# Kernel optimization log

Hardware: AMD Instinct MI355X
Metric: run time of the kernel (lower is better)

Reference implementation:

```python
import jax, jax.numpy as jnp
import numpy as np

B, T, C = 4, 2048, 1024
H, HKV, D = 8, 4, 128          # query heads, kv heads, head dim (C = H*D)
RATIO = 4                       # csa_compress_ratio -> block size
G = T // RATIO                  # number of compressed blocks (T divisible by RATIO)
HI, DI = 8, 64                  # indexer heads / head dim
TOPK = 64                       # index_topk blocks selected per query
ROPE_DIM = 64                   # partial RoPE applied to last ROPE_DIM dims of D
THETA = 160000.0                # compress_rope_theta
RANK = 512                      # grouped output projection rank (o_groups=1)
NEG = -1e30


def rmsnorm(x):
    return x * jax.lax.rsqrt(jnp.mean(jnp.square(x), axis=-1, keepdims=True) + 1e-6)


def rope_tables(pos):
    half = ROPE_DIM // 2
    inv_freq = 1.0 / (THETA ** (jnp.arange(half, dtype=jnp.float32) / half))
    ang = pos.astype(jnp.float32)[:, None] * inv_freq[None, :]   # [P, half]
    return jnp.cos(ang), jnp.sin(ang)


def partial_rope(x, cos, sin):
    # x: [..., P, heads, D]; rotate only the last ROPE_DIM dims
    x_nope, x_rope = x[..., :-ROPE_DIM], x[..., -ROPE_DIM:]
    x1, x2 = jnp.split(x_rope, 2, axis=-1)
    c = cos[:, None, :]  # [P,1,half] broadcast over heads
    s = sin[:, None, :]
    rot = jnp.concatenate([x1 * c - x2 * s, x1 * s + x2 * c], axis=-1)
    return jnp.concatenate([x_nope, rot], axis=-1)


def gated_compress(x, Wk, Wv, Wg, ape, n_head, head_dim):
    # Learned gated softmax pooling over fixed blocks of RATIO tokens.
    k = (x @ Wk).reshape(B, G, RATIO, n_head, head_dim)
    v = (x @ Wv).reshape(B, G, RATIO, n_head, head_dim)
    g = (x @ Wg).reshape(B, G, RATIO, n_head, head_dim) + ape[None, None]
    w = jax.nn.softmax(g, axis=2)
    return (k * w).sum(axis=2), (v * w).sum(axis=2)  # [B,G,h,d]


def setup_inputs() -> dict:
    key = jax.random.key(0)
    ks = jax.random.split(key, 11)
    s = 0.02
    def w(k, shape):
        return jax.random.normal(k, shape, jnp.float32) * s
    return {
        "x": jax.random.normal(ks[0], (B, T, C), jnp.float32),
        "Wq": w(ks[1], (C, H * D)),
        "Wck": w(ks[2], (C, HKV * D)),
        "Wcv": w(ks[3], (C, HKV * D)),
        "Wcg": w(ks[4], (C, HKV * D)),
        "ape_c": jnp.zeros((RATIO, HKV, D), jnp.float32),
        "Wiq": w(ks[5], (C, HI * DI)),
        "Wik": w(ks[6], (C, HI * DI)),
        "Wig": w(ks[7], (C, HI * DI)),
        "ape_i": jnp.zeros((RATIO, HI, DI), jnp.float32),
        "Wa": w(ks[8], (1, RANK, C)),
        "Wb": w(ks[9], (RANK, C)),
    }


def reference(x, Wq, Wck, Wcv, Wcg, ape_c, Wiq, Wik, Wig, ape_i, Wa, Wb):
    group_ends = jnp.arange(RATIO - 1, T, RATIO)                 # [G]
    causal = group_ends[None, :] <= jnp.arange(T)[:, None]       # [T,G]

    # --- LightningIndexer: select TOPK compressed blocks per query token ---
    ki = (x @ Wik).reshape(B, G, RATIO, HI, DI)
    gi = (x @ Wig).reshape(B, G, RATIO, HI, DI) + ape_i[None, None]
    wi = jax.nn.softmax(gi, axis=2)
    ikeys = rmsnorm((ki * wi).sum(axis=2))                       # [B,G,HI,DI]
    iq = rmsnorm((x @ Wiq).reshape(B, T, HI, DI))
    isc = jnp.einsum('bthd,bghd->bhtg', iq, ikeys) * (DI ** -0.5)
    isc = isc.mean(axis=1)                                       # [B,T,G]
    isc = jnp.where(causal[None], isc, NEG)
    sel = jax.lax.top_k(isc, TOPK)[1]                            # [B,T,TOPK]
    mask = jnp.zeros((B, T, G), dtype=bool).at[
        jnp.arange(B)[:, None, None], jnp.arange(T)[None, :, None], sel
    ].set(True)
    mask = mask & causal[None]                                   # [B,T,G]

    # --- Compressed KV + partial RoPE ---
    ck, cv = gated_compress(x, Wck, Wcv, Wcg, ape_c, HKV, D)     # [B,G,HKV,D]
    cos_q, sin_q = rope_tables(jnp.arange(T))
    cos_k, sin_k = rope_tables(group_ends)
    q = partial_rope((x @ Wq).reshape(B, T, H, D), cos_q, sin_q)
    ck = partial_rope(ck, cos_k, sin_k)

    # --- GQA attention over selected compressed blocks ---
    rep = H // HKV
    ck_r = jnp.repeat(ck, rep, axis=2)                           # [B,G,H,D]
    cv_r = jnp.repeat(cv, rep, axis=2)
    scores = jnp.einsum('bthd,bghd->bhtg', q, ck_r) * (D ** -0.5)
    m = mask[:, None]                                            # [B,1,T,G]
    attw = jax.nn.softmax(jnp.where(m, scores, NEG), axis=-1) * m
    attn = jnp.einsum('bhtg,bghd->bthd', attw, cv_r).reshape(B, T, C)

    # --- GroupedOutputProjection (o_groups=1, low-rank) ---
    r = jnp.einsum('btgd,grd->btgr', attn.reshape(B, T, 1, C), Wa).reshape(B, T, RANK)
    return rmsnorm(r) @ Wb
```

## Files before the change

kernel.cpp:

```cpp
#include <hip/hip_runtime.h>
#include <hip/hip_bf16.h>
#include <math.h>

constexpr int kB = 4, kT = 2048, kC = 1024;
constexpr int kH = 8, kHKV = 4, kD = 128;
constexpr int kRATIO = 4, kG = 512;
constexpr int kHI = 8, kDI = 64;
constexpr int kTOPK = 64, kRANK = 512;
constexpr float kTHETA = 160000.0f;
constexpr float kNEG = -1e30f;

constexpr int NTOT = 2560;
constexpr int Q_OFF = 0;
constexpr int CK_OFF = 1024;
constexpr int CV_OFF = 1536;
constexpr int CG_OFF = 2048;

constexpr int PLD = 1536;
constexpr int P_IQ = 0, P_KI = 512, P_GI = 1024;

typedef short short8 __attribute__((ext_vector_type(8)));
typedef float floatx4 __attribute__((ext_vector_type(4)));

__device__ inline float waveReduceSum(float v) {
    #pragma unroll
    for (int m = 32; m > 0; m >>= 1) v += __shfl_xor(v, m, 64);
    return v;
}
__device__ inline double waveReduceSumD(double v) {
    #pragma unroll
    for (int m = 32; m > 0; m >>= 1) v += __shfl_xor(v, m, 64);
    return v;
}
__device__ inline float waveReduceMax(float v) {
    #pragma unroll
    for (int m = 32; m > 0; m >>= 1) v = fmaxf(v, __shfl_xor(v, m, 64));
    return v;
}

__device__ inline unsigned short f2bf(float f) {
    union { float f; unsigned int u; } v; v.f = f;
    unsigned int r = v.u + 0x7FFFu + ((v.u >> 16) & 1u);
    return (unsigned short)(r >> 16);
}
__device__ inline float bf2f(unsigned short h) {
    union { unsigned int u; float f; } v; v.u = ((unsigned int)h) << 16;
    return v.f;
}

__global__ __launch_bounds__(256) void split_rows_kernel(
    const float* __restrict__ in, unsigned short* __restrict__ out,
    int K, int kshift, const float* __restrict__ rowScale)
{
    int idx = blockIdx.x * 256 + threadIdx.x;
    int row = idx >> kshift;
    int kc = (idx & ((1 << kshift) - 1)) << 2;
    float4 v = *(const float4*)(in + (size_t)row * K + kc);
    if (rowScale) {
        float s = rowScale[row];
        v.x *= s; v.y *= s; v.z *= s; v.w *= s;
    }
    unsigned short h[4], l[4];
    float vv[4] = {v.x, v.y, v.z, v.w};
    #pragma unroll
    for (int i = 0; i < 4; ++i) {
        h[i] = f2bf(vv[i]);
        l[i] = f2bf(vv[i] - bf2f(h[i]));
    }
    size_t ob = (size_t)row * (2 * K);
    uint2 hw, lw;
    hw.x = (unsigned)h[0] | ((unsigned)h[1] << 16);
    hw.y = (unsigned)h[2] | ((unsigned)h[3] << 16);
    lw.x = (unsigned)l[0] | ((unsigned)l[1] << 16);
    lw.y = (unsigned)l[2] | ((unsigned)l[3] << 16);
    *(uint2*)(out + ob + kc) = hw;
    *(uint2*)(out + ob + K + kc) = lw;
}

__global__ __launch_bounds__(256) void transpose_split_kernel(
    const float* __restrict__ W, int N, int K, unsigned short* __restrict__ Wt)
{
    __shared__ float Ws[64][68];
    int k0 = blockIdx.x * 64, n0 = blockIdx.y * 64;
    int tid = threadIdx.x;
    #pragma unroll
    for (int it = 0; it < 4; ++it) {
        int krow = (tid >> 4) + it * 16;
        float4 v = *(const float4*)(W + (size_t)(k0 + krow) * N + n0 + (tid & 15) * 4);
        *(float4*)&Ws[krow][(tid & 15) * 4] = v;
    }
    __syncthreads();
    #pragma unroll
    for (int it = 0; it < 2; ++it) {
        int idx = tid + it * 256;
        int nrow = idx >> 3;
        int kc8 = (idx & 7) * 8;
        unsigned short h[8], l[8];
        #pragma unroll
        for (int j = 0; j < 8; ++j) {
            float v = Ws[kc8 + j][nrow];
            h[j] = f2bf(v);
            l[j] = f2bf(v - bf2f(h[j]));
        }
        size_t ob = (size_t)(n0 + nrow) * (2 * K) + k0;
        uint4 hw, lw;
        hw.x = (unsigned)h[0] | ((unsigned)h[1] << 16);
        hw.y = (unsigned)h[2] | ((unsigned)h[3] << 16);
        hw.z = (unsigned)h[4] | ((unsigned)h[5] << 16);
        hw.w = (unsigned)h[6] | ((unsigned)h[7] << 16);
        lw.x = (unsigned)l[0] | ((unsigned)l[1] << 16);
        lw.y = (unsigned)l[2] | ((unsigned)l[3] << 16);
        lw.z = (unsigned)l[4] | ((unsigned)l[5] << 16);
        lw.w = (unsigned)l[6] | ((unsigned)l[7] << 16);
        *(uint4*)(Wt + ob + kc8) = hw;
        *(uint4*)(Wt + ob + K + kc8) = lw;
    }
}

#define TSTRIDE 40

__global__ __launch_bounds__(256) void gemm_mfma_kernel(
    const unsigned short* __restrict__ A,
    const unsigned short* __restrict__ B,
    float* __restrict__ C, int ldc, int Kin)
{
    __shared__ unsigned short As[128 * TSTRIDE];
    __shared__ unsigned short Bs[128 * TSTRIDE];
    const int tid = threadIdx.x;
    const int n0 = blockIdx.x * 128, m0 = blockIdx.y * 128;
    const int w = tid >> 6, lane = tid & 63;
    const int q = lane >> 4, r = lane & 15;
    const int wm = (w & 1) * 64, wn = (w >> 1) * 64;
    const int lda = 2 * Kin, ldb = 2 * Kin;
    const int srow = tid >> 2;
    const int sko = (tid & 3) * 8;

    floatx4 acc[4][4] = {};
    const int KT = 3 * Kin;
    for (int k0 = 0; k0 < KT; k0 += 32) {
        int ka = (k0 < 2 * Kin) ? k0 : k0 - 2 * Kin;
        int kb = (k0 < Kin) ? k0 : k0 - Kin;
        __syncthreads();
        #pragma unroll
        for (int rep = 0; rep < 2; ++rep) {
            int row = srow + rep * 64;
            uint4 av = *(const uint4*)(A + (size_t)(m0 + row) * lda + ka + sko);
            uint4 bv = *(const uint4*)(B + (size_t)(n0 + row) * ldb + kb + sko);
            *(uint4*)&As[row * TSTRIDE + sko] = av;
            *(uint4*)&Bs[row * TSTRIDE + sko] = bv;
        }
        __syncthreads();
        short8 af[4], bf[4];
        #pragma unroll
        for (int i = 0; i < 4; ++i)
            af[i] = *(const short8*)&As[(wm + i * 16 + r) * TSTRIDE + q * 8];
        #pragma unroll
        for (int j = 0; j < 4; ++j)
            bf[j] = *(const short8*)&Bs[(wn + j * 16 + r) * TSTRIDE + q * 8];
        #pragma unroll
        for (int i = 0; i < 4; ++i)
            #pragma unroll
            for (int j = 0; j < 4; ++j)
                acc[i][j] = __builtin_amdgcn_mfma_f32_16x16x32_bf16(
                    af[i], bf[j], acc[i][j], 0, 0, 0);
    }
    #pragma unroll
    for (int i = 0; i < 4; ++i)
        #pragma unroll
        for (int j = 0; j < 4; ++j)
            #pragma unroll
            for (int reg = 0; reg < 4; ++reg)
                C[(size_t)(m0 + wm + i * 16 + q * 4 + reg) * ldc
                  + n0 + wn + j * 16 + r] = acc[i][j][reg];
}

__global__ __launch_bounds__(256) void rope_q_kernel(float* __restrict__ Y)
{
    int idx = blockIdx.x * 256 + threadIdx.x;
    int j = idx & 31;
    int rest = idx >> 5;
    int h = rest & 7;  rest >>= 3;
    int t = rest & (kT - 1);
    int b = rest >> 11;
    size_t base = (size_t)(b * kT + t) * NTOT + Q_OFF + h * kD;
    float inv_freq = powf(kTHETA, -(float)j * (1.0f / 32.0f));
    float ang = (float)t * inv_freq;
    float c = cosf(ang), s = sinf(ang);
    float x1 = Y[base + 64 + j];
    float x2 = Y[base + 96 + j];
    Y[base + 64 + j] = x1 * c - x2 * s;
    Y[base + 96 + j] = x1 * s + x2 * c;
}

__global__ __launch_bounds__(128) void compress_c_kernel(
    const float* __restrict__ Y, const float* __restrict__ ape_c,
    float* __restrict__ ck, float* __restrict__ cv)
{
    int bid = blockIdx.x;
    int h = bid & 3;
    int g = (bid >> 2) & (kG - 1);
    int b = bid >> 11;
    int d = threadIdx.x;
    float kv[kRATIO], vv[kRATIO], gv[kRATIO];
    #pragma unroll
    for (int r = 0; r < kRATIO; ++r) {
        size_t row = (size_t)(b * kT + g * kRATIO + r) * NTOT;
        kv[r] = Y[row + CK_OFF + h * kD + d];
        vv[r] = Y[row + CV_OFF + h * kD + d];
        gv[r] = Y[row + CG_OFF + h * kD + d] + ape_c[(r * kHKV + h) * kD + d];
    }
    float m = fmaxf(fmaxf(gv[0], gv[1]), fmaxf(gv[2], gv[3]));
    float ka = 0.f, va = 0.f, den = 0.f;
    #pragma unroll
    for (int r = 0; r < kRATIO; ++r) {
        float e = expf(gv[r] - m);
        den += e;
        ka += kv[r] * e;
        va += vv[r] * e;
    }
    ka /= den; va /= den;
    size_t obase = ((size_t)(b * kG + g) * kHKV + h) * kD;
    cv[obase + d] = va;
    __shared__ float cks[kD];
    cks[d] = ka;
    __syncthreads();
    int pos = 4 * g + 3;
    float out;
    if (d < 64) {
        out = cks[d];
    } else if (d < 96) {
        int j = d - 64;
        float inv_freq = powf(kTHETA, -(float)j * (1.0f / 32.0f));
        float ang = (float)pos * inv_freq;
        out = cks[d] * cosf(ang) - cks[d + 32] * sinf(ang);
    } else {
        int j = d - 96;
        float inv_freq = powf(kTHETA, -(float)j * (1.0f / 32.0f));
        float ang = (float)pos * inv_freq;
        out = cks[d - 32] * sinf(ang) + cks[d] * cosf(ang);
    }
    ck[obase + d] = out;
}

__global__ __launch_bounds__(256) void concat_w_kernel(
    const float* __restrict__ Wiq, const float* __restrict__ Wik,
    const float* __restrict__ Wig, float* __restrict__ Wcat)
{
    int idx = blockIdx.x * 256 + threadIdx.x;
    int row = idx / 384;
    int col = (idx - row * 384) * 4;
    float4 v;
    if (col < 512)       v = *(const float4*)(Wiq + (size_t)row * 512 + col);
    else if (col < 1024) v = *(const float4*)(Wik + (size_t)row * 512 + col - 512);
    else                 v = *(const float4*)(Wig + (size_t)row * 512 + col - 1024);
    *(float4*)(Wcat + (size_t)row * PLD + col) = v;
}

__global__ __launch_bounds__(256) void proj_f64_kernel(
    const float* __restrict__ x, const float* __restrict__ W,
    double* __restrict__ P)
{
    __shared__ double As[16][65];
    __shared__ double Bs[16][68];
    const int tid = threadIdx.x;
    const int bx = blockIdx.x, by = blockIdx.y;
    const int tx = tid & 15, ty = tid >> 4;
    const int arow = tid >> 2;
    const int akq  = (tid & 3) << 2;
    const int brow = tid >> 4;
    const int bcol = (tid & 15) << 2;
    const float* Ap = x + (size_t)(by * 64 + arow) * kC + akq;
    const float* Bp = W + (size_t)brow * PLD + bx * 64 + bcol;
    double acc[4][4] = {};
    for (int k0 = 0; k0 < kC; k0 += 16) {
        float4 a4 = *(const float4*)(Ap + k0);
        float4 b4 = *(const float4*)(Bp + (size_t)k0 * PLD);
        __syncthreads();
        As[akq + 0][arow] = (double)a4.x;
        As[akq + 1][arow] = (double)a4.y;
        As[akq + 2][arow] = (double)a4.z;
        As[akq + 3][arow] = (double)a4.w;
        Bs[brow][bcol + 0] = (double)b4.x;
        Bs[brow][bcol + 1] = (double)b4.y;
        Bs[brow][bcol + 2] = (double)b4.z;
        Bs[brow][bcol + 3] = (double)b4.w;
        __syncthreads();
        #pragma unroll
        for (int kk = 0; kk < 16; ++kk) {
            double a[4];
            #pragma unroll
            for (int i = 0; i < 4; ++i) a[i] = As[kk][ty * 4 + i];
            #pragma unroll
            for (int j = 0; j < 4; ++j) {
                double bv = Bs[kk][tx * 4 + j];
                #pragma unroll
                for (int i = 0; i < 4; ++i)
                    acc[i][j] = fma(a[i], bv, acc[i][j]);
            }
        }
    }
    #pragma unroll
    for (int i = 0; i < 4; ++i)
        #pragma unroll
        for (int j = 0; j < 4; ++j)
            P[(size_t)(by * 64 + ty * 4 + i) * PLD + bx * 64 + tx * 4 + j] = acc[i][j];
}

__global__ __launch_bounds__(64) void gate_i_kernel(
    const double* __restrict__ P, const float* __restrict__ ape_i,
    double* __restrict__ ikeys64)
{
    int bid = blockIdx.x;
    int h = bid & 7;
    int g = (bid >> 3) & (kG - 1);
    int b = bid >> 12;
    int lane = threadIdx.x;
    double kk[kRATIO], gg[kRATIO];
    #pragma unroll
    for (int r = 0; r < kRATIO; ++r) {
        size_t row = (size_t)(b * kT + g * kRATIO + r) * PLD;
        kk[r] = P[row + P_KI + h * kDI + lane];
        gg[r] = P[row + P_GI + h * kDI + lane] + (double)ape_i[(r * kHI + h) * kDI + lane];
    }
    double m = fmax(fmax(gg[0], gg[1]), fmax(gg[2], gg[3]));
    double acc = 0.0, den = 0.0;
    #pragma unroll
    for (int r = 0; r < kRATIO; ++r) {
        double e = exp(gg[r] - m);
        den += e;
        acc += kk[r] * e;
    }
    acc /= den;
    double ss = waveReduceSumD(acc * acc);
    double scale = 1.0 / sqrt(ss * (1.0 / kDI) + 1e-6);
    ikeys64[((size_t)(b * kG + g) * kHI + h) * kDI + lane] = acc * scale;
}

__global__ __launch_bounds__(512) void rmsiq64_kernel(double* __restrict__ P)
{
    int row = blockIdx.x;
    int tid = threadIdx.x;
    double* p = P + (size_t)row * PLD + P_IQ + tid;
    double v = *p;
    double ss = v * v;
    #pragma unroll
    for (int m = 32; m > 0; m >>= 1) ss += __shfl_xor(ss, m, 64);
    double scale = 1.0 / sqrt(ss * (1.0 / kDI) + 1e-6);
    *p = v * scale;
}

#define BM 64
#define BN 64
#define BK 16

__global__ __launch_bounds__(256) void isc_f64_kernel(
    const double* __restrict__ P, const double* __restrict__ ikeys64,
    double* __restrict__ isc64)
{
    __shared__ double As[BK][BM + 1];
    __shared__ double Bs[BK][BN + 4];
    const int tid = threadIdx.x;
    const int bx = blockIdx.x, by = blockIdx.y;
    const int b = by >> 5;
    const int tx = tid & 15, ty = tid >> 4;
    const int arow = tid >> 2;
    const int akq  = (tid & 3) << 2;
    const double* Ap = P + (size_t)(by * BM + arow) * PLD + P_IQ + akq;
    const double* Bp = ikeys64 + (size_t)b * kG * 512 + (size_t)(bx * BN + arow) * 512 + akq;
    double acc[4][4] = {};
    for (int k0 = 0; k0 < 512; k0 += BK) {
        double a0 = Ap[k0], a1 = Ap[k0 + 1], a2 = Ap[k0 + 2], a3 = Ap[k0 + 3];
        double b0 = Bp[k0], b1 = Bp[k0 + 1], b2 = Bp[k0 + 2], b3 = Bp[k0 + 3];
        __syncthreads();
        As[akq + 0][arow] = a0; As[akq + 1][arow] = a1;
        As[akq + 2][arow] = a2; As[akq + 3][arow] = a3;
        Bs[akq + 0][arow] = b0; Bs[akq + 1][arow] = b1;
        Bs[akq + 2][arow] = b2; Bs[akq + 3][arow] = b3;
        __syncthreads();
        #pragma unroll
        for (int kk = 0; kk < BK; ++kk) {
            double a[4];
            #pragma unroll
            for (int i = 0; i < 4; ++i) a[i] = As[kk][ty * 4 + i];
            #pragma unroll
            for (int j = 0; j < 4; ++j) {
                double bv = Bs[kk][tx * 4 + j];
                #pragma unroll
                for (int i = 0; i < 4; ++i)
                    acc[i][j] = fma(a[i], bv, acc[i][j]);
            }
        }
    }
    #pragma unroll
    for (int i = 0; i < 4; ++i)
        #pragma unroll
        for (int j = 0; j < 4; ++j)
            isc64[(size_t)(by * BM + ty * 4 + i) * kG + bx * BN + tx * 4 + j] =
                acc[i][j] * (1.0 / 64.0);
}

__global__ __launch_bounds__(256) void topk_kernel(
    const double* __restrict__ isc, int* __restrict__ sel, int* __restrict__ cnt)
{
    int bt = blockIdx.x;
    int t = bt & (kT - 1);
    int tid = threadIdx.x;
    __shared__ double sv[kG];
    __shared__ int si[kG];
    const double* row = isc + (size_t)bt * kG;
    for (int g = tid; g < kG; g += 256) {
        bool causal = (4 * g + 3) <= t;
        sv[g] = causal ? row[g] : (double)kNEG;
        si[g] = g;
    }
    __syncthreads();
    for (int k = 2; k <= kG; k <<= 1) {
        for (int j = k >> 1; j > 0; j >>= 1) {
            for (int i = tid; i < kG; i += 256) {
                int l = i ^ j;
                if (l > i) {
                    double vi = sv[i], vl = sv[l];
                    int ii = si[i], il = si[l];
                    bool l_first = (vl > vi) || (vl == vi && il < ii);
                    bool desc = ((i & k) == 0);
                    if (desc ? l_first : !l_first) {
                        sv[i] = vl; sv[l] = vi;
                        si[i] = il; si[l] = ii;
                    }
                }
            }
            __syncthreads();
        }
    }
    int count = (t >= 3) ? (((t - 3) >> 2) + 1) : 0;
    int n = count < kTOPK ? count : kTOPK;
    if (tid < kTOPK) sel[(size_t)bt * kTOPK + tid] = (tid < n) ? si[tid] : 0;
    if (tid == 0) cnt[bt] = n;
}

__global__ __launch_bounds__(64) void attn_kernel(
    const float* __restrict__ Y, const float* __restrict__ ck,
    const float* __restrict__ cv, const int* __restrict__ sel,
    const int* __restrict__ cnt, unsigned short* __restrict__ acat)
{
    int bid = blockIdx.x;
    int h = bid & 7;
    int row = bid >> 3;
    int b = row >> 11;
    int lane = threadIdx.x;
    __shared__ float qs[kD];
    __shared__ float ws[kTOPK];
    __shared__ int gs[kTOPK];
    const float* qp = Y + (size_t)row * NTOT + Q_OFF + h * kD;
    qs[lane] = qp[lane];
    qs[lane + 64] = qp[lane + 64];
    __syncthreads();
    int n = cnt[row];
    unsigned short* outp = acat + (size_t)row * 2048 + h * kD;
    float acc0 = 0.f, acc1 = 0.f;
    if (n > 0) {
        int kvh = h >> 1;
        float score = kNEG;
        int g = 0;
        if (lane < n) {
            g = sel[(size_t)row * kTOPK + lane];
            const float* ckp = ck + ((size_t)(b * kG + g) * kHKV + kvh) * kD;
            float s = 0.f;
            #pragma unroll
            for (int d = 0; d < kD; d += 4) {
                float4 c4 = *(const float4*)(ckp + d);
                s += qs[d] * c4.x + qs[d + 1] * c4.y + qs[d + 2] * c4.z + qs[d + 3] * c4.w;
            }
            score = s * 0.08838834764831845f;
        }
        float m = waveReduceMax(score);
        float p = (lane < n) ? expf(score - m) : 0.f;
        float sum = waveReduceSum(p);
        float w = p / sum;
        ws[lane] = w;
        gs[lane] = g;
        __syncthreads();
        for (int j = 0; j < n; ++j) {
            float wj = ws[j];
            const float* cvp = cv + ((size_t)(b * kG + gs[j]) * kHKV + kvh) * kD;
            acc0 = fmaf(wj, cvp[lane], acc0);
            acc1 = fmaf(wj, cvp[lane + 64], acc1);
        }
    }
    unsigned short h0 = f2bf(acc0), h1 = f2bf(acc1);
    outp[lane] = h0;
    outp[lane + 64] = h1;
    outp[1024 + lane] = f2bf(acc0 - bf2f(h0));
    outp[1024 + lane + 64] = f2bf(acc1 - bf2f(h1));
}

__global__ __launch_bounds__(64) void rms_rows_kernel(
    const float* __restrict__ R, float* __restrict__ scale)
{
    int row = blockIdx.x;
    int lane = threadIdx.x;
    const float* p = R + (size_t)row * kRANK;
    float s = 0.f;
    #pragma unroll
    for (int i = 0; i < kRANK / 64; ++i) {
        float v = p[lane + i * 64];
        s = fmaf(v, v, s);
    }
    s = waveReduceSum(s);
    if (lane == 0) scale[row] = 1.0f / sqrtf(s * (1.0f / kRANK) + 1e-6f);
}

extern "C" void kernel_launch(void* const* d_in, const int* in_sizes, int n_in,
                              void* d_out, int out_size, void* d_ws, size_t ws_size,
                              hipStream_t stream)
{
    const float* x    = (const float*)d_in[0];
    const float* Wq   = (const float*)d_in[1];
    const float* Wck  = (const float*)d_in[2];
    const float* Wcv  = (const float*)d_in[3];
    const float* Wcg  = (const float*)d_in[4];
    const float* ape_c= (const float*)d_in[5];
    const float* Wiq  = (const float*)d_in[6];
    const float* Wik  = (const float*)d_in[7];
    const float* Wig  = (const float*)d_in[8];
    const float* ape_i= (const float*)d_in[9];
    const float* Wa   = (const float*)d_in[10];
    const float* Wb   = (const float*)d_in[11];
    float* out = (float*)d_out;

    const int M = kB * kT;

    char* p = (char*)d_ws;
    double* P       = (double*)p;              p += (size_t)M * PLD * 8;
    double* ikeys64 = (double*)p;              p += (size_t)kB * kG * 512 * 8;
    double* isc64   = (double*)p;              p += (size_t)M * kG * 8;
    float* ck       = (float*)p;               p += (size_t)kB * kG * kHKV * kD * 4;
    float* cv       = (float*)p;               p += (size_t)kB * kG * kHKV * kD * 4;
    float* rbuf     = (float*)p;               p += (size_t)M * kRANK * 4;
    float* rscale   = (float*)p;               p += (size_t)M * 4;
    int* sel        = (int*)p;                 p += (size_t)M * kTOPK * 4;
    int* cnt        = (int*)p;                 p += (size_t)M * 4;
    unsigned short* xcat  = (unsigned short*)p; p += (size_t)M * 2048 * 2;
    unsigned short* Wtall = (unsigned short*)p; p += (size_t)NTOT * 2048 * 2;
    unsigned short* Wat   = (unsigned short*)p; p += (size_t)kRANK * 2048 * 2;
    unsigned short* Wbt   = (unsigned short*)p; p += (size_t)kC * 1024 * 2;
    float* Wcat     = (float*)p;               p += (size_t)kC * PLD * 4;
    float* Y = (float*)P;
    unsigned short* acat  = xcat;
    unsigned short* rncat = (unsigned short*)isc64;

    concat_w_kernel<<<(kC * PLD / 4) / 256, 256, 0, stream>>>(Wiq, Wik, Wig, Wcat);
    proj_f64_kernel<<<dim3(PLD / 64, M / 64), 256, 0, stream>>>(x, Wcat, P);
    gate_i_kernel<<<kB * kG * kHI, 64, 0, stream>>>(P, ape_i, ikeys64);
    rmsiq64_kernel<<<M, 512, 0, stream>>>(P);
    isc_f64_kernel<<<dim3(kG / BN, M / BM), 256, 0, stream>>>(P, ikeys64, isc64);
    topk_kernel<<<kB * kT, 256, 0, stream>>>(isc64, sel, cnt);

    split_rows_kernel<<<(size_t)M * kC / 4 / 256, 256, 0, stream>>>(
        x, xcat, kC, 8, nullptr);
    transpose_split_kernel<<<dim3(kC / 64, 1024 / 64), 256, 0, stream>>>(
        Wq, 1024, kC, Wtall + (size_t)Q_OFF * 2048);
    transpose_split_kernel<<<dim3(kC / 64, 512 / 64), 256, 0, stream>>>(
        Wck, 512, kC, Wtall + (size_t)CK_OFF * 2048);
    transpose_split_kernel<<<dim3(kC / 64, 512 / 64), 256, 0, stream>>>(
        Wcv, 512, kC, Wtall + (size_t)CV_OFF * 2048);
    transpose_split_kernel<<<dim3(kC / 64, 512 / 64), 256, 0, stream>>>(
        Wcg, 512, kC, Wtall + (size_t)CG_OFF * 2048);

    gemm_mfma_kernel<<<dim3(NTOT / 128, M / 128), 256, 0, stream>>>(
        xcat, Wtall, Y, NTOT, kC);

    rope_q_kernel<<<(kB * kT * kH * 32) / 256, 256, 0, stream>>>(Y);
    compress_c_kernel<<<kB * kG * kHKV, 128, 0, stream>>>(Y, ape_c, ck, cv);

    attn_kernel<<<kB * kT * kH, 64, 0, stream>>>(Y, ck, cv, sel, cnt, acat);

    split_rows_kernel<<<(size_t)kRANK * kC / 4 / 256, 256, 0, stream>>>(
        Wa, Wat, kC, 8, nullptr);
    gemm_mfma_kernel<<<dim3(kRANK / 128, M / 128), 256, 0, stream>>>(
        acat, Wat, rbuf, kRANK, kC);

    rms_rows_kernel<<<M, 64, 0, stream>>>(rbuf, rscale);
    split_rows_kernel<<<(size_t)M * kRANK / 4 / 256, 256, 0, stream>>>(
        rbuf, rncat, kRANK, 7, rscale);
    transpose_split_kernel<<<dim3(kRANK / 64, kC / 64), 256, 0, stream>>>(
        Wb, kC, kRANK, Wbt);
    gemm_mfma_kernel<<<dim3(kC / 128, M / 128), 256, 0, stream>>>(
        rncat, Wbt, out, kC, kRANK);

    (void)in_sizes; (void)n_in; (void)out_size; (void)ws_size;
}
```

Before: 1.795 ms.

## Enlarge f64 projection tile and pack topk sort into single 64-bit keys

```diff
diff --git a/kernel.cpp b/kernel.cpp
--- a/kernel.cpp
+++ b/kernel.cpp
@@ -256,54 +256,64 @@
     *(float4*)(Wcat + (size_t)row * PLD + col) = v;
 }
 
+#define PBM 128
+#define PBN 64
+#define PBK 16
+
 __global__ __launch_bounds__(256) void proj_f64_kernel(
     const float* __restrict__ x, const float* __restrict__ W,
     double* __restrict__ P)
 {
-    __shared__ double As[16][65];
-    __shared__ double Bs[16][68];
+    __shared__ double As[PBK][129];
+    __shared__ double Bs[PBK][68];
     const int tid = threadIdx.x;
     const int bx = blockIdx.x, by = blockIdx.y;
     const int tx = tid & 15, ty = tid >> 4;
-    const int arow = tid >> 2;
-    const int akq  = (tid & 3) << 2;
-    const int brow = tid >> 4;
-    const int bcol = (tid & 15) << 2;
-    const float* Ap = x + (size_t)(by * 64 + arow) * kC + akq;
-    const float* Bp = W + (size_t)brow * PLD + bx * 64 + bcol;
-    double acc[4][4] = {};
-    for (int k0 = 0; k0 < kC; k0 += 16) {
-        float4 a4 = *(const float4*)(Ap + k0);
-        float4 b4 = *(const float4*)(Bp + (size_t)k0 * PLD);
+    const int ar = tid >> 1;
+    const int ak = (tid & 1) * 8;
+    const int br = tid >> 4;
+    const int bc = tid & 15;
+    const float* Ap = x + (size_t)(by * PBM + ar) * kC + ak;
+    const float* Bp = W + (size_t)br * PLD + bx * PBN + bc;
+    double acc[8][4] = {};
+    for (int k0 = 0; k0 < kC; k0 += PBK) {
+        float4 a0 = *(const float4*)(Ap + k0);
+        float4 a1 = *(const float4*)(Ap + k0 + 4);
+        const float* bp = Bp + (size_t)k0 * PLD;
+        float b0 = bp[0], b1 = bp[16], b2 = bp[32], b3 = bp[48];
         __syncthreads();
-        As[akq + 0][arow] = (double)a4.x;
-        As[akq + 1][arow] = (double)a4.y;
-        As[akq + 2][arow] = (double)a4.z;
-        As[akq + 3][arow] = (double)a4.w;
-        Bs[brow][bcol + 0] = (double)b4.x;
-        Bs[brow][bcol + 1] = (double)b4.y;
-        Bs[brow][bcol + 2] = (double)b4.z;
-        Bs[brow][bcol + 3] = (double)b4.w;
+        As[ak + 0][ar] = (double)a0.x;
+        As[ak + 1][ar] = (double)a0.y;
+        As[ak + 2][ar] = (double)a0.z;
+        As[ak + 3][ar] = (double)a0.w;
+        As[ak + 4][ar] = (double)a1.x;
+        As[ak + 5][ar] = (double)a1.y;
+        As[ak + 6][ar] = (double)a1.z;
+        As[ak + 7][ar] = (double)a1.w;
+        Bs[br][bc]      = (double)b0;
+        Bs[br][bc + 16] = (double)b1;
+        Bs[br][bc + 32] = (double)b2;
+        Bs[br][bc + 48] = (double)b3;
         __syncthreads();
         #pragma unroll
-        for (int kk = 0; kk < 16; ++kk) {
-            double a[4];
-            #pragma unroll
-            for (int i = 0; i < 4; ++i) a[i] = As[kk][ty * 4 + i];
-            #pragma unroll
-            for (int j = 0; j < 4; ++j) {
-                double bv = Bs[kk][tx * 4 + j];
+        for (int kk = 0; kk < PBK; ++kk) {
+            double a[8], b[4];
+            #pragma unroll
+            for (int i = 0; i < 8; ++i) a[i] = As[kk][ty * 8 + i];
+            #pragma unroll
+            for (int j = 0; j < 4; ++j) b[j] = Bs[kk][tx + 16 * j];
+            #pragma unroll
+            for (int i = 0; i < 8; ++i)
                 #pragma unroll
-                for (int i = 0; i < 4; ++i)
-                    acc[i][j] = fma(a[i], bv, acc[i][j]);
-            }
-        }
-    }
-    #pragma unroll
-    for (int i = 0; i < 4; ++i)
+                for (int j = 0; j < 4; ++j)
+                    acc[i][j] = fma(a[i], b[j], acc[i][j]);
+        }
+    }
+    #pragma unroll
+    for (int i = 0; i < 8; ++i)
         #pragma unroll
         for (int j = 0; j < 4; ++j)
-            P[(size_t)(by * 64 + ty * 4 + i) * PLD + bx * 64 + tx * 4 + j] = acc[i][j];
+            P[(size_t)(by * PBM + ty * 8 + i) * PLD + bx * PBN + tx + 16 * j] = acc[i][j];
 }
 
 __global__ __launch_bounds__(64) void gate_i_kernel(
@@ -405,27 +415,33 @@
     int bt = blockIdx.x;
     int t = bt & (kT - 1);
     int tid = threadIdx.x;
-    __shared__ double sv[kG];
-    __shared__ int si[kG];
+    __shared__ unsigned long long sk[kG];
     const double* row = isc + (size_t)bt * kG;
     for (int g = tid; g < kG; g += 256) {
         bool causal = (4 * g + 3) <= t;
-        sv[g] = causal ? row[g] : (double)kNEG;
-        si[g] = g;
+        unsigned long long key;
+        if (causal) {
+            union { double d; unsigned long long u; } v; v.d = row[g];
+            unsigned long long b = v.u;
+            key = (b >> 63) ? ~b : (b | 0x8000000000000000ULL);
+            key = (key & ~511ULL) | (unsigned long long)(511 - g);
+        } else {
+            key = (unsigned long long)(511 - g);
+        }
+        sk[g] = key;
     }
     __syncthreads();
     for (int k = 2; k <= kG; k <<= 1) {
         for (int j = k >> 1; j > 0; j >>= 1) {
+            #pragma unroll 2
             for (int i = tid; i < kG; i += 256) {
                 int l = i ^ j;
                 if (l > i) {
-                    double vi = sv[i], vl = sv[l];
-                    int ii = si[i], il = si[l];
-                    bool l_first = (vl > vi) || (vl == vi && il < ii);
+                    unsigned long long ki = sk[i], kl = sk[l];
+                    bool l_first = kl > ki;
                     bool desc = ((i & k) == 0);
                     if (desc ? l_first : !l_first) {
-                        sv[i] = vl; sv[l] = vi;
-                        si[i] = il; si[l] = ii;
+                        sk[i] = kl; sk[l] = ki;
                     }
                 }
             }
@@ -434,7 +450,9 @@
     }
     int count = (t >= 3) ? (((t - 3) >> 2) + 1) : 0;
     int n = count < kTOPK ? count : kTOPK;
-    if (tid < kTOPK) sel[(size_t)bt * kTOPK + tid] = (tid < n) ? si[tid] : 0;
+    if (tid < kTOPK)
+        sel[(size_t)bt * kTOPK + tid] =
+            (tid < n) ? (511 - (int)(sk[tid] & 511ULL)) : 0;
     if (tid == 0) cnt[bt] = n;
 }
 
@@ -550,7 +568,7 @@
     unsigned short* rncat = (unsigned short*)isc64;
 
     concat_w_kernel<<<(kC * PLD / 4) / 256, 256, 0, stream>>>(Wiq, Wik, Wig, Wcat);
-    proj_f64_kernel<<<dim3(PLD / 64, M / 64), 256, 0, stream>>>(x, Wcat, P);
+    proj_f64_kernel<<<dim3(PLD / PBN, M / PBM), 256, 0, stream>>>(x, Wcat, P);
     gate_i_kernel<<<kB * kG * kHI, 64, 0, stream>>>(P, ape_i, ikeys64);
     rmsiq64_kernel<<<M, 512, 0, stream>>>(P);
     isc_f64_kernel<<<dim3(kG / BN, M / BM), 256, 0, stream>>>(P, ikeys64, isc64);
```

New measurement: 1.567 ms. -12.7%, faster.
